# Kernel optimization log

Hardware: AMD Instinct MI355X
Metric: run time of the kernel (lower is better)

The kernel has to match this reference:

```python
import jax, jax.numpy as jnp
import numpy as np
import math

B, S, D, H = 4, 2048, 1024, 16
HD = D // H  # head_dim = 64


def setup_inputs() -> dict:
    key = jax.random.key(0)
    ks = jax.random.split(key, 5)
    x = jax.random.normal(ks[0], (B, S, D), dtype=jnp.float32)
    # causal mask, broadcastable over batch and heads
    mask = jnp.tril(jnp.ones((S, S), dtype=bool))[None, None]
    # Linear params in [in, out] layout (math-equivalent to torch's [out, in])
    w_attn = jax.random.normal(ks[1], (D, 3 * D), dtype=jnp.float32) * (1.0 / math.sqrt(D))
    b_attn = jax.random.normal(ks[2], (3 * D,), dtype=jnp.float32) * 0.02
    w_proj = jax.random.normal(ks[3], (D, D), dtype=jnp.float32) * (1.0 / math.sqrt(D))
    b_proj = jax.random.normal(ks[4], (D,), dtype=jnp.float32) * 0.02
    return {"x": x, "mask": mask, "w_attn": w_attn, "b_attn": b_attn,
            "w_proj": w_proj, "b_proj": b_proj}


def reference(x, mask, w_attn, b_attn, w_proj, b_proj):
    b, s, d = x.shape
    # fused qkv projection, then split heads -> [b, h, s, hd]
    qkv = x @ w_attn + b_attn
    q, k, v = jnp.split(qkv, 3, axis=-1)
    split = lambda t: t.reshape(b, s, H, HD).transpose(0, 2, 1, 3)
    q, k, v = split(q), split(k), split(v)
    # scaled dot-product attention with boolean mask (True = keep)
    scores = jnp.einsum('bhqd,bhkd->bhqk', q, k) / math.sqrt(HD)
    scores = jnp.where(mask, scores, -jnp.inf)
    attn = jax.nn.softmax(scores, axis=-1)  # attn_dropout with p=0 is identity
    out = jnp.einsum('bhqk,bhkd->bhqd', attn, v)
    out = out.transpose(0, 2, 1, 3).reshape(b, s, d)
    # output projection (resid_dropout with p=0 is identity)
    return out @ w_proj + b_proj
```

## Files before the change

kernel.cpp:

```cpp
#include <hip/hip_runtime.h>

typedef unsigned short u16;
typedef __attribute__((ext_vector_type(4))) float floatx4;
typedef __attribute__((ext_vector_type(8))) short shortx8;

#define B_ 4
#define S_ 2048
#define D_ 1024
#define H_ 16
#define HD_ 64

__device__ __forceinline__ float b2f(u16 u) {
    return __uint_as_float(((unsigned int)u) << 16);
}
__device__ __forceinline__ u16 f2b(float f) {
    unsigned int u = __float_as_uint(f);
    u += 0x7fffu + ((u >> 16) & 1u);
    return (u16)(u >> 16);
}
__device__ __forceinline__ unsigned long long pack4(float a, float b, float c, float d) {
    return (unsigned long long)f2b(a) | ((unsigned long long)f2b(b) << 16) |
           ((unsigned long long)f2b(c) << 32) | ((unsigned long long)f2b(d) << 48);
}
__device__ __forceinline__ unsigned int permpk(float a, float b) {
    return __builtin_amdgcn_perm(__float_as_uint(b) + 0x8000u,
                                 __float_as_uint(a) + 0x8000u, 0x07060302u);
}
__device__ __forceinline__ void glds16(const u16* g, u16* l) {
    __builtin_amdgcn_global_load_lds(
        (const __attribute__((address_space(1))) unsigned int*)g,
        (__attribute__((address_space(3))) unsigned int*)l, 16, 0, 0);
}
__device__ __forceinline__ void bar() {
    asm volatile("" ::: "memory");
    __builtin_amdgcn_s_barrier();
    asm volatile("" ::: "memory");
}
#define VMW4 asm volatile("s_waitcnt vmcnt(4)" ::: "memory")
#define VMW0 asm volatile("s_waitcnt vmcnt(0)" ::: "memory")

__global__ __launch_bounds__(256) void preproc(const void* __restrict__ xin,
                                               u16* __restrict__ xb,
                                               const void* __restrict__ bA,
                                               const void* __restrict__ bP,
                                               u16* __restrict__ bAb,
                                               u16* __restrict__ bPb,
                                               const void* __restrict__ wA,
                                               u16* __restrict__ wtA,
                                               const void* __restrict__ wP,
                                               u16* __restrict__ wtP,
                                               int* __restrict__ flag) {
    __shared__ int cnts[4];
    __shared__ u16 tile[32][33];
    const int tid = threadIdx.x;
    {
        const unsigned int e = (((const unsigned int*)xin)[tid] >> 7) & 0xffu;
        int c = (e >= 110u && e <= 134u) ? 1 : 0;
#pragma unroll
        for (int d = 1; d < 64; d <<= 1) c += __shfl_xor(c, d);
        if ((tid & 63) == 0) cnts[tid >> 6] = c;
    }
    __syncthreads();
    const int isbf = (cnts[0] + cnts[1] + cnts[2] + cnts[3] > 128) ? 1 : 0;

    const int bid = blockIdx.x;
    if (bid < 4096) {
        const size_t i = ((size_t)bid * 256 + tid) * 8;
        if (isbf) {
            *(uint4*)(xb + i) = *(const uint4*)((const u16*)xin + i);
        } else {
            const float* xf = (const float*)xin;
            float4 a = *(const float4*)(xf + i);
            float4 b = *(const float4*)(xf + i + 4);
            u16 o[8] = {f2b(a.x), f2b(a.y), f2b(a.z), f2b(a.w),
                        f2b(b.x), f2b(b.y), f2b(b.z), f2b(b.w)};
            *(uint4*)(xb + i) = *(uint4*)o;
        }
        if (bid == 0) {
            if (tid == 0) *flag = isbf;
            for (int j = tid; j < 3072; j += 256)
                bAb[j] = isbf ? ((const u16*)bA)[j] : f2b(((const float*)bA)[j]);
            for (int j = tid; j < 1024; j += 256)
                bPb[j] = isbf ? ((const u16*)bP)[j] : f2b(((const float*)bP)[j]);
        }
    } else {
        const int idx = bid - 4096;
        int bxi = idx & 127;
        const int by = (idx >> 7) * 32;
        const void* in;
        u16* out;
        int N;
        if (bxi < 96) { in = wA; out = wtA; N = 3072; }
        else          { in = wP; out = wtP; N = 1024; bxi -= 96; }
        const int K = 1024;
        const int bx = bxi * 32;
        const int tx = tid & 31;
        const int ty = tid >> 5;
        if (isbf) {
#pragma unroll
            for (int i = 0; i < 32; i += 8)
                tile[ty + i][tx] = ((const u16*)in)[(size_t)(by + ty + i) * N + bx + tx];
        } else {
#pragma unroll
            for (int i = 0; i < 32; i += 8)
                tile[ty + i][tx] = f2b(((const float*)in)[(size_t)(by + ty + i) * N + bx + tx]);
        }
        __syncthreads();
#pragma unroll
        for (int i = 0; i < 32; i += 8)
            out[(size_t)(bx + ty + i) * K + by + tx] = tile[tx][ty + i];
    }
}

template <int MODE>
__global__ __launch_bounds__(256) void gemm_bt(const u16* __restrict__ A,
                                               const u16* __restrict__ BT,
                                               const u16* __restrict__ bias,
                                               void* __restrict__ outv,
                                               int M, int N, int K,
                                               u16* __restrict__ qws,
                                               u16* __restrict__ kws,
                                               u16* __restrict__ vws,
                                               const int* __restrict__ flag) {
    __shared__ __align__(16) u16 As[3][128 * 32];
    __shared__ __align__(16) u16 Bs[3][128 * 32];

    const int isbf = (MODE == 0) ? *flag : 1;
    const int tid = threadIdx.x;
    const int w = tid >> 6, l = tid & 63;
    const int lane_m = l & 15, quad = l >> 4;
    const int bid = blockIdx.x;
    const int bm = ((bid & 7) * 8 + ((bid >> 3) & 7)) * 128;
    const int bn = (bid >> 6) * 128;
    const int wm = (w >> 1) * 64, wn = (w & 1) * 64;

    floatx4 acc[4][4];
#pragma unroll
    for (int i = 0; i < 4; i++)
#pragma unroll
        for (int j = 0; j < 4; j++) acc[i][j] = (floatx4){0.f, 0.f, 0.f, 0.f};

    const int lr = l >> 2, sl = l & 3;
    const int cA = sl ^ ((lr >> 1) & 3);
    const int rb0 = w * 16, rb1 = 64 + w * 16;
    const u16* Arow0 = A + (size_t)(bm + rb0 + lr) * K + cA * 8;
    const u16* Arow1 = A + (size_t)(bm + rb1 + lr) * K + cA * 8;
    const u16* Brow0 = BT + (size_t)(bn + rb0 + lr) * K + cA * 8;
    const u16* Brow1 = BT + (size_t)(bn + rb1 + lr) * K + cA * 8;

    auto stage = [&](int t) {
        const int k0 = t * 32;
        u16* ad = &As[t % 3][0];
        u16* bd = &Bs[t % 3][0];
        glds16(Arow0 + k0, ad + rb0 * 32);
        glds16(Arow1 + k0, ad + rb1 * 32);
        glds16(Brow0 + k0, bd + rb0 * 32);
        glds16(Brow1 + k0, bd + rb1 * 32);
    };

    const int NT = K >> 5;
    stage(0);
    stage(1);
    for (int t = 0; t < NT; ++t) {
        if (t < NT - 1) { VMW4; } else { VMW0; }
        bar();
        if (t + 2 < NT) stage(t + 2);

        const u16* Ac = &As[t % 3][0];
        const u16* Bc = &Bs[t % 3][0];
        shortx8 af[4], bf[4];
#pragma unroll
        for (int mb = 0; mb < 4; mb++) {
            const int r = wm + mb * 16 + lane_m;
            af[mb] = *(const shortx8*)(Ac + r * 32 + (quad ^ ((r >> 1) & 3)) * 8);
        }
#pragma unroll
        for (int nb = 0; nb < 4; nb++) {
            const int r = wn + nb * 16 + lane_m;
            bf[nb] = *(const shortx8*)(Bc + r * 32 + (quad ^ ((r >> 1) & 3)) * 8);
        }
#pragma unroll
        for (int mb = 0; mb < 4; mb++)
#pragma unroll
            for (int nb = 0; nb < 4; nb++)
                acc[mb][nb] = __builtin_amdgcn_mfma_f32_16x16x32_bf16(
                    af[mb], bf[nb], acc[mb][nb], 0, 0, 0);
    }

    const float SCALE_Q = 0.18033688011112042f;

    if (MODE == 1 && (bn >> 10) == 2) {
        __syncthreads();
        u16* ep = (w < 2) ? &As[w][0] : &Bs[w - 2][0];
#pragma unroll
        for (int nb = 0; nb < 4; nb++) {
            const int lhd = nb * 16 + lane_m;
            const float bv = b2f(bias[bn + wn + lhd]);
            const int sw = (lhd & 7) << 3;
#pragma unroll
            for (int mb = 0; mb < 4; mb++) {
                const int o = mb * 16 + quad * 4;
                unsigned long long pk =
                    pack4(acc[mb][nb][0] + bv, acc[mb][nb][1] + bv,
                          acc[mb][nb][2] + bv, acc[mb][nb][3] + bv);
                *(unsigned long long*)(ep + lhd * 64 + (o ^ sw)) = pk;
            }
        }
        __syncthreads();
        const int bI = bm >> 11;
        const int hI = ((bn + wn) >> 6) & 15;
        const int s0 = (bm & 2047) + wm;
        u16* vb0 = vws + (size_t)(bI * 16 + hI) * 64 * 2048;
        const int rr8 = l >> 3, c8 = l & 7;
#pragma unroll
        for (int p = 0; p < 8; p++) {
            const int lhd = p * 8 + rr8;
            uint4 v4 = *(const uint4*)(ep + lhd * 64 + ((c8 << 3) ^ ((lhd & 7) << 3)));
            *(uint4*)(vb0 + (size_t)lhd * 2048 + s0 + c8 * 8) = v4;
        }
    } else {
#pragma unroll
        for (int nb = 0; nb < 4; nb++) {
            const int col = bn + wn + nb * 16 + lane_m;
            const float bv = b2f(bias[col]);
#pragma unroll
            for (int mb = 0; mb < 4; mb++) {
                const int rowb = bm + wm + mb * 16 + quad * 4;
#pragma unroll
                for (int r = 0; r < 4; r++) {
                    float v = acc[mb][nb][r] + bv;
                    const int rr = rowb + r;
                    if (MODE == 0) {
                        if (isbf) ((u16*)outv)[(size_t)rr * N + col] = f2b(v);
                        else ((float*)outv)[(size_t)rr * N + col] = v;
                    } else {
                        const int which = col >> 10;
                        if (which == 0) v *= SCALE_Q;
                        const int h = (col >> 6) & 15;
                        const int hd = col & 63;
                        const int b = rr >> 11, s = rr & 2047;
                        u16* dst = which == 0 ? qws : kws;
                        dst[((size_t)(b * 16 + h) * 2048 + s) * 64 + hd] = f2b(v);
                    }
                }
            }
        }
    }
}

__global__ __launch_bounds__(512, 4) void attn_kernel(const u16* __restrict__ Qg,
                                                      const u16* __restrict__ Kg,
                                                      const u16* __restrict__ Vtg,
                                                      u16* __restrict__ Og) {
    __shared__ __align__(16) u16 Ks[2][64 * 64];
    __shared__ __align__(16) u16 Vs[2][64 * 64];
    __shared__ __align__(16) u16 Ps[8][16 * 72];

    const int tid = threadIdx.x, w = tid >> 6, l = tid & 63;
    const int lane_m = l & 15, quad = l >> 4;
    const int bid = blockIdx.x;
    const int bh = (bid & 7) * 8 + ((bid >> 3) >> 3);
    const int xmi = (bid >> 3) & 7;
    const u16* qp = Qg + (size_t)bh * S_ * 64;
    const u16* kp = Kg + (size_t)bh * S_ * 64;
    const u16* vtp = Vtg + (size_t)bh * 64 * S_;
    u16* psw = &Ps[w][0];
    const int b = bh >> 4, h = bh & 15;

    const int lr8 = l >> 3, sl8 = l & 7;
    const int cK = sl8 ^ (lr8 & 7);
    const int rbase = w * 8;
    const u16* Kr = kp + (size_t)(rbase + lr8) * 64 + cK * 8;
    const u16* Vr = vtp + (size_t)(rbase + lr8) * S_ + cK * 8;

    auto stage = [&](int t) {
        const int k0 = t * 64;
        glds16(Kr + (size_t)k0 * 64, &Ks[t & 1][0] + rbase * 64);
        glds16(Vr + k0, &Vs[t & 1][0] + rbase * 64);
    };

    for (int pass = 0; pass < 2; pass++) {
        const int xm = pass ? (15 - xmi) : xmi;
        const int q0 = xm * 128;
        const int qw0 = q0 + w * 16;

        shortx8 qF[2];
#pragma unroll
        for (int ks = 0; ks < 2; ks++)
            qF[ks] = *(const shortx8*)(qp + (size_t)(qw0 + lane_m) * 64 + ks * 32 + quad * 8);

        floatx4 o_acc[4];
#pragma unroll
        for (int md = 0; md < 4; md++) o_acc[md] = (floatx4){0.f, 0.f, 0.f, 0.f};
        float m_i = -1e30f, l_i = 0.f;

        const int ntiles = (q0 >> 6) + 2;
        const int myend = qw0 + 15;

        __syncthreads();
        stage(0);
        for (int t = 0; t < ntiles; t++) {
            const int k0 = t * 64;
            __syncthreads();
            if (t + 1 < ntiles) stage(t + 1);

            if (k0 <= myend) {
                const u16* kb = &Ks[t & 1][0];
                const u16* vb = &Vs[t & 1][0];
                floatx4 sc[4];
#pragma unroll
                for (int mb = 0; mb < 4; mb++) sc[mb] = (floatx4){0.f, 0.f, 0.f, 0.f};
#pragma unroll
                for (int ks = 0; ks < 2; ks++) {
                    shortx8 kA[4];
#pragma unroll
                    for (int mb = 0; mb < 4; mb++) {
                        const int r = mb * 16 + lane_m;
                        kA[mb] = *(const shortx8*)(kb + r * 64 + (((ks * 4 + quad) ^ (r & 7)) * 8));
                    }
                    __builtin_amdgcn_s_setprio(1);
#pragma unroll
                    for (int mb = 0; mb < 4; mb++)
                        sc[mb] = __builtin_amdgcn_mfma_f32_16x16x32_bf16(
                            kA[mb], qF[ks], sc[mb], 0, 0, 0);
                    __builtin_amdgcn_s_setprio(0);
                }

                const int qg = qw0 + lane_m;
                if (k0 + 63 > qw0) {
#pragma unroll
                    for (int mb = 0; mb < 4; mb++)
#pragma unroll
                        for (int r = 0; r < 4; r++) {
                            const int kvg = k0 + mb * 16 + quad * 4 + r;
                            if (kvg > qg) sc[mb][r] = -1e30f;
                        }
                }
                float mloc = -1e30f;
#pragma unroll
                for (int mb = 0; mb < 4; mb++) {
                    float a = fmaxf(fmaxf(sc[mb][0], sc[mb][1]),
                                    fmaxf(sc[mb][2], sc[mb][3]));
                    mloc = fmaxf(mloc, a);
                }
                mloc = fmaxf(mloc, __shfl_xor(mloc, 16));
                mloc = fmaxf(mloc, __shfl_xor(mloc, 32));
                float mnew = m_i;
                if (!__all(mloc <= m_i + 8.0f)) {
                    mnew = fmaxf(m_i, mloc);
                    const float alpha = __builtin_amdgcn_exp2f(m_i - mnew);
                    m_i = mnew;
                    l_i *= alpha;
#pragma unroll
                    for (int md = 0; md < 4; md++) o_acc[md] *= alpha;
                }
                float psum = 0.f;
#pragma unroll
                for (int mb = 0; mb < 4; mb++) {
                    const float p0 = __builtin_amdgcn_exp2f(sc[mb][0] - mnew);
                    const float p1 = __builtin_amdgcn_exp2f(sc[mb][1] - mnew);
                    const float p2 = __builtin_amdgcn_exp2f(sc[mb][2] - mnew);
                    const float p3 = __builtin_amdgcn_exp2f(sc[mb][3] - mnew);
                    psum += (p0 + p1) + (p2 + p3);
                    uint2 pk = {permpk(p0, p1), permpk(p2, p3)};
                    *(uint2*)(psw + lane_m * 72 + mb * 16 + quad * 4) = pk;
                }
                psum += __shfl_xor(psum, 16);
                psum += __shfl_xor(psum, 32);
                l_i += psum;

#pragma unroll
                for (int ks = 0; ks < 2; ks++) {
                    shortx8 vF[4], pF;
#pragma unroll
                    for (int md = 0; md < 4; md++) {
                        const int r = md * 16 + lane_m;
                        vF[md] = *(const shortx8*)(vb + r * 64 + (((ks * 4 + quad) ^ (r & 7)) * 8));
                    }
                    pF = *(const shortx8*)(psw + lane_m * 72 + ks * 32 + quad * 8);
                    __builtin_amdgcn_s_setprio(1);
#pragma unroll
                    for (int md = 0; md < 4; md++)
                        o_acc[md] = __builtin_amdgcn_mfma_f32_16x16x32_bf16(
                            vF[md], pF, o_acc[md], 0, 0, 0);
                    __builtin_amdgcn_s_setprio(0);
                }
            }
        }

        {
            const float inv = 1.0f / l_i;
            const int qg = qw0 + lane_m;
            const size_t base = ((size_t)b * 2048 + qg) * 1024 + h * 64;
#pragma unroll
            for (int md = 0; md < 4; md++) {
                *(unsigned long long*)(Og + base + md * 16 + quad * 4) =
                    pack4(o_acc[md][0] * inv, o_acc[md][1] * inv,
                          o_acc[md][2] * inv, o_acc[md][3] * inv);
            }
        }
    }
}

extern "C" void kernel_launch(void* const* d_in, const int* in_sizes, int n_in,
                              void* d_out, int out_size, void* d_ws, size_t ws_size,
                              hipStream_t stream) {
    const void* x      = d_in[0];
    const void* w_attn = d_in[2];
    const void* b_attn = d_in[3];
    const void* w_proj = d_in[4];
    const void* b_proj = d_in[5];

    u16* qws = (u16*)d_ws;
    u16* kws = qws + 8388608;
    u16* vws = kws + 8388608;
    u16* xb  = vws + 8388608;
    u16* aws = xb;
    u16* wtA = xb + 8388608;
    u16* wtP = wtA + 3145728;
    u16* bAb = wtP + 1048576;
    u16* bPb = bAb + 3072;
    int* flag = (int*)(bPb + 1024);

    preproc<<<8192, 256, 0, stream>>>(x, xb, b_attn, b_proj, bAb, bPb,
                                      w_attn, wtA, w_proj, wtP, flag);

    gemm_bt<1><<<dim3(64 * 24), 256, 0, stream>>>(
        xb, wtA, bAb, nullptr, 8192, 3072, 1024, qws, kws, vws, flag);

    attn_kernel<<<dim3(512), 512, 0, stream>>>(qws, kws, vws, aws);

    gemm_bt<0><<<dim3(64 * 8), 256, 0, stream>>>(
        aws, wtP, bPb, d_out, 8192, 1024, 1024, nullptr, nullptr, nullptr, flag);
}
```

Measured before the change: 274.2 us.

## Enlarge GEMM block tile to 256x128 with eight warps per block

```diff
diff --git a/kernel.cpp b/kernel.cpp
--- a/kernel.cpp
+++ b/kernel.cpp
@@ -36,7 +36,7 @@
     __builtin_amdgcn_s_barrier();
     asm volatile("" ::: "memory");
 }
-#define VMW4 asm volatile("s_waitcnt vmcnt(4)" ::: "memory")
+#define VMW3 asm volatile("s_waitcnt vmcnt(3)" ::: "memory")
 #define VMW0 asm volatile("s_waitcnt vmcnt(0)" ::: "memory")
 
 __global__ __launch_bounds__(256) void preproc(const void* __restrict__ xin,
@@ -113,7 +113,7 @@
 }
 
 template <int MODE>
-__global__ __launch_bounds__(256) void gemm_bt(const u16* __restrict__ A,
+__global__ __launch_bounds__(512) void gemm_bt(const u16* __restrict__ A,
                                                const u16* __restrict__ BT,
                                                const u16* __restrict__ bias,
                                                void* __restrict__ outv,
@@ -122,16 +122,15 @@
                                                u16* __restrict__ kws,
                                                u16* __restrict__ vws,
                                                const int* __restrict__ flag) {
-    __shared__ __align__(16) u16 As[3][128 * 32];
-    __shared__ __align__(16) u16 Bs[3][128 * 32];
+    __shared__ __align__(16) u16 lds[36864];
 
     const int isbf = (MODE == 0) ? *flag : 1;
     const int tid = threadIdx.x;
     const int w = tid >> 6, l = tid & 63;
     const int lane_m = l & 15, quad = l >> 4;
     const int bid = blockIdx.x;
-    const int bm = ((bid & 7) * 8 + ((bid >> 3) & 7)) * 128;
-    const int bn = (bid >> 6) * 128;
+    const int bm = ((bid & 7) * 4 + ((bid >> 3) & 3)) * 256;
+    const int bn = (bid >> 5) * 128;
     const int wm = (w >> 1) * 64, wn = (w & 1) * 64;
 
     floatx4 acc[4][4];
@@ -142,32 +141,30 @@
 
     const int lr = l >> 2, sl = l & 3;
     const int cA = sl ^ ((lr >> 1) & 3);
-    const int rb0 = w * 16, rb1 = 64 + w * 16;
-    const u16* Arow0 = A + (size_t)(bm + rb0 + lr) * K + cA * 8;
-    const u16* Arow1 = A + (size_t)(bm + rb1 + lr) * K + cA * 8;
-    const u16* Brow0 = BT + (size_t)(bn + rb0 + lr) * K + cA * 8;
-    const u16* Brow1 = BT + (size_t)(bn + rb1 + lr) * K + cA * 8;
+    const int ra0 = w * 32, ra1 = w * 32 + 16, rb = w * 16;
+    const u16* Arow0 = A + (size_t)(bm + ra0 + lr) * K + cA * 8;
+    const u16* Arow1 = A + (size_t)(bm + ra1 + lr) * K + cA * 8;
+    const u16* Brow  = BT + (size_t)(bn + rb + lr) * K + cA * 8;
 
     auto stage = [&](int t) {
         const int k0 = t * 32;
-        u16* ad = &As[t % 3][0];
-        u16* bd = &Bs[t % 3][0];
-        glds16(Arow0 + k0, ad + rb0 * 32);
-        glds16(Arow1 + k0, ad + rb1 * 32);
-        glds16(Brow0 + k0, bd + rb0 * 32);
-        glds16(Brow1 + k0, bd + rb1 * 32);
+        u16* ad = lds + (t % 3) * 8192;
+        u16* bd = lds + 24576 + (t % 3) * 4096;
+        glds16(Arow0 + k0, ad + ra0 * 32);
+        glds16(Arow1 + k0, ad + ra1 * 32);
+        glds16(Brow + k0, bd + rb * 32);
     };
 
     const int NT = K >> 5;
     stage(0);
     stage(1);
     for (int t = 0; t < NT; ++t) {
-        if (t < NT - 1) { VMW4; } else { VMW0; }
+        if (t < NT - 1) { VMW3; } else { VMW0; }
         bar();
         if (t + 2 < NT) stage(t + 2);
 
-        const u16* Ac = &As[t % 3][0];
-        const u16* Bc = &Bs[t % 3][0];
+        const u16* Ac = lds + (t % 3) * 8192;
+        const u16* Bc = lds + 24576 + (t % 3) * 4096;
         shortx8 af[4], bf[4];
 #pragma unroll
         for (int mb = 0; mb < 4; mb++) {
@@ -191,7 +188,7 @@
 
     if (MODE == 1 && (bn >> 10) == 2) {
         __syncthreads();
-        u16* ep = (w < 2) ? &As[w][0] : &Bs[w - 2][0];
+        u16* ep = lds + w * 4096;
 #pragma unroll
         for (int nb = 0; nb < 4; nb++) {
             const int lhd = nb * 16 + lane_m;
@@ -425,11 +422,11 @@
     preproc<<<8192, 256, 0, stream>>>(x, xb, b_attn, b_proj, bAb, bPb,
                                       w_attn, wtA, w_proj, wtP, flag);
 
-    gemm_bt<1><<<dim3(64 * 24), 256, 0, stream>>>(
+    gemm_bt<1><<<dim3(32 * 24), 512, 0, stream>>>(
         xb, wtA, bAb, nullptr, 8192, 3072, 1024, qws, kws, vws, flag);
 
     attn_kernel<<<dim3(512), 512, 0, stream>>>(qws, kws, vws, aws);
 
-    gemm_bt<0><<<dim3(64 * 8), 256, 0, stream>>>(
+    gemm_bt<0><<<dim3(32 * 8), 512, 0, stream>>>(
         aws, wtP, bPb, d_out, 8192, 1024, 1024, nullptr, nullptr, nullptr, flag);
 }
```

Measured after the change: 260.3 us. -5.1%, faster.
